# Kernel tuning notes

Hardware: AMD Instinct MI355X
Metric: run time of the kernel (lower is better)

Reference implementation:

```python
import jax, jax.numpy as jnp
import numpy as np

DIM = 1024
HIDDEN = 4096
N_EXPERTS = 8
K = 2
TEMP = 1.0


def setup_inputs() -> dict:
    key = jax.random.key(0)
    ks = jax.random.split(key, 7)
    s = 0.02
    x = jax.random.normal(ks[0], (4, 2048, DIM), dtype=jnp.float32)
    router_w = jax.random.normal(ks[1], (N_EXPERTS, DIM), dtype=jnp.float32) * s
    router_b = jnp.zeros((N_EXPERTS,), dtype=jnp.float32)
    # Expert(dim, hidden, 'swiglu'): fc1: dim -> 2*hidden, fc2: hidden -> dim
    w1 = jax.random.normal(ks[2], (N_EXPERTS, 2 * HIDDEN, DIM), dtype=jnp.float32) * s
    b1 = jnp.zeros((N_EXPERTS, 2 * HIDDEN), dtype=jnp.float32)
    w2 = jax.random.normal(ks[3], (N_EXPERTS, DIM, HIDDEN), dtype=jnp.float32) * s
    b2 = jnp.zeros((N_EXPERTS, DIM), dtype=jnp.float32)
    return {"x": x, "router_w": router_w, "router_b": router_b,
            "w1": w1, "b1": b1, "w2": w2, "b2": b2}


def _expert_ffn(xf, wa, ba, wb, bb):
    # xf: [T, dim]; swiglu FFN
    h = xf @ wa.T + ba                       # [T, 2*hidden]
    h1, h2 = jnp.split(h, 2, axis=-1)
    h = jax.nn.silu(h1) * h2                 # [T, hidden]
    return h @ wb.T + bb                     # [T, dim]


def reference(x, router_w, router_b, w1, b1, w2, b2):
    b, t, d = x.shape
    logits = (x @ router_w.T + router_b) / TEMP          # [b, t, E]
    topk_val, topk_idx = jax.lax.top_k(logits, K)        # [b, t, K]
    weights = jax.nn.softmax(topk_val, axis=-1)          # [b, t, K]

    xf = x.reshape(-1, d)                                # [T, dim]
    # Compute every expert on all tokens (dense reference for irregular dispatch)
    outs = jax.vmap(_expert_ffn, in_axes=(None, 0, 0, 0, 0))(xf, w1, b1, w2, b2)  # [E, T, dim]
    outs = jnp.transpose(outs, (1, 0, 2))                # [T, E, dim]

    idx = topk_idx.reshape(-1, K)                        # [T, K]
    gathered = jnp.take_along_axis(outs, idx[:, :, None], axis=1)  # [T, K, dim]
    combined = (gathered * weights.reshape(-1, K, 1)).sum(axis=1)  # [T, dim]
    return combined.reshape(b, t, d)
```

## Files before the change

kernel.cpp:

```cpp
#include <hip/hip_runtime.h>

#define T_TOK 8192
#define DIMX 1024
#define HID 4096
#define NE 8
#define TP (T_TOK * 2)
#define PADR 128
#define BK 64

typedef unsigned short ushort_t;
typedef __attribute__((ext_vector_type(4))) float f32x4;
typedef __attribute__((ext_vector_type(8))) short bf16x8;

__device__ __forceinline__ ushort_t f2bf(float f) {
    unsigned u = __float_as_uint(f);
    u += 0x7FFFu + ((u >> 16) & 1u);
    return (ushort_t)(u >> 16);
}
__device__ __forceinline__ float b2f(ushort_t h) {
    return __uint_as_float(((unsigned)h) << 16);
}

__device__ __forceinline__ void gload_lds16(const void* g, void* l) {
    __builtin_amdgcn_global_load_lds((const __attribute__((address_space(1))) void*)g,
                                     (__attribute__((address_space(3))) void*)l, 16, 0, 0);
}

__device__ __forceinline__ f32x4 mfma16(bf16x8 a, bf16x8 b, f32x4 c) {
    return __builtin_amdgcn_mfma_f32_16x16x32_bf16(a, b, c, 0, 0, 0);
}


__global__ void zero_kernel(int* p) {
    if (threadIdx.x < 16) p[threadIdx.x] = 0;
}

__global__ __launch_bounds__(256) void router_kernel(
    const float* __restrict__ x, const float* __restrict__ rw, const float* __restrict__ rb,
    int* __restrict__ counts, int* __restrict__ topk_idx, float* __restrict__ topk_w)
{
    __shared__ float s_rw[NE * DIMX];
    int tid = threadIdx.x;
    for (int i = tid * 4; i < NE * DIMX; i += 1024) {
        float4 v = *(const float4*)(rw + i);
        *(float4*)(s_rw + i) = v;
    }
    __syncthreads();
    int lane = tid & 63, wid = tid >> 6;
    int t = blockIdx.x * 4 + wid;
    const float* xr = x + (size_t)t * DIMX;
    float acc[NE];
#pragma unroll
    for (int e = 0; e < NE; e++) acc[e] = 0.f;
    for (int j = 0; j < DIMX; j += 64) {
        float xv = xr[j + lane];
#pragma unroll
        for (int e = 0; e < NE; e++) acc[e] += xv * s_rw[e * DIMX + j + lane];
    }
#pragma unroll
    for (int e = 0; e < NE; e++) {
#pragma unroll
        for (int off = 32; off > 0; off >>= 1) acc[e] += __shfl_xor(acc[e], off, 64);
    }
    if (lane == 0) {
        float v[NE];
#pragma unroll
        for (int e = 0; e < NE; e++) v[e] = acc[e] + rb[e];
        int i0 = 0; float b0 = v[0];
#pragma unroll
        for (int e = 1; e < NE; e++) if (v[e] > b0) { b0 = v[e]; i0 = e; }
        int i1 = -1; float b1v = -1e30f;
#pragma unroll
        for (int e = 0; e < NE; e++) if (e != i0 && v[e] > b1v) { b1v = v[e]; i1 = e; }
        float ex = __expf(b1v - b0);
        float inv = 1.f / (1.f + ex);
        topk_idx[t * 2]     = i0;  topk_idx[t * 2 + 1] = i1;
        topk_w[t * 2]       = inv; topk_w[t * 2 + 1]   = ex * inv;
        atomicAdd(&counts[i0], 1); atomicAdd(&counts[i1], 1);
    }
}

__global__ void prefix_kernel(const int* __restrict__ counts, int* __restrict__ offsets) {
    if (threadIdx.x == 0 && blockIdx.x == 0) {
        int s = 0;
        for (int e = 0; e < NE; e++) { offsets[e] = s; s += counts[e]; }
    }
}

__global__ __launch_bounds__(256) void scatter_kernel(
    const int* __restrict__ topk_idx, const float* __restrict__ topk_w,
    const int* __restrict__ offsets, int* __restrict__ cursor,
    int* __restrict__ tok_of, float* __restrict__ w_of, int* __restrict__ slot_of)
{
    int i = blockIdx.x * 256 + threadIdx.x;
    int e = topk_idx[i];
    int pos = offsets[e] + atomicAdd(&cursor[e], 1);
    tok_of[pos] = i >> 1;
    w_of[pos] = topk_w[i];
    slot_of[i] = pos;
}


__global__ __launch_bounds__(256) void cvt_kernel(
    const float* __restrict__ src, ushort_t* __restrict__ dst, int n8)
{
    int i = blockIdx.x * 256 + threadIdx.x;
    if (i >= n8) return;
    float4 a = ((const float4*)src)[i * 2];
    float4 b = ((const float4*)src)[i * 2 + 1];
    ushort4 lo = make_ushort4(f2bf(a.x), f2bf(a.y), f2bf(a.z), f2bf(a.w));
    ushort4 hi = make_ushort4(f2bf(b.x), f2bf(b.y), f2bf(b.z), f2bf(b.w));
    ((ushort4*)dst)[i * 2] = lo;
    ((ushort4*)dst)[i * 2 + 1] = hi;
}

__global__ __launch_bounds__(256) void gather_kernel(
    const float* __restrict__ x, const int* __restrict__ tok_of, ushort_t* __restrict__ Xp)
{
    int pos = blockIdx.x;
    int t = tok_of[pos];
    int i = threadIdx.x;
    float4 v = ((const float4*)(x + (size_t)t * DIMX))[i];
    ushort4 o = make_ushort4(f2bf(v.x), f2bf(v.y), f2bf(v.z), f2bf(v.w));
    ((ushort4*)(Xp + (size_t)pos * DIMX))[i] = o;
}

__global__ __launch_bounds__(256, 2) void fc1_kernel(
    const ushort_t* __restrict__ Xp, const ushort_t* __restrict__ w1b,
    const float* __restrict__ b1,
    const int* __restrict__ counts, const int* __restrict__ offsets,
    ushort_t* __restrict__ H)
{
    const int e = blockIdx.z, mt = blockIdx.y, nt = blockIdx.x;
    const int cnt = counts[e];
    if (mt * 128 >= cnt) return;
    const int base = offsets[e] + mt * 128;
    int rows_valid = cnt - mt * 128; if (rows_valid > 128) rows_valid = 128;

    __shared__ ushort_t As[128 * BK];
    __shared__ ushort_t Bs1[64 * BK];
    __shared__ ushort_t Bs2[64 * BK];

    const int tid = threadIdx.x, lane = tid & 63, wid = tid >> 6;
    const int wave_m = wid >> 1, wave_n = wid & 1;

    const ushort_t* Ag  = Xp + (size_t)base * DIMX;
    const ushort_t* B1g = w1b + ((size_t)e * 2 * HID + (size_t)nt * 64) * DIMX;
    const ushort_t* B2g = B1g + (size_t)HID * DIMX;

    const ushort_t* agp[4]; ushort_t* alp[4];
#pragma unroll
    for (int i = 0; i < 4; i++) {
        int s = wid * 4 + i;
        int r = s * 8 + (lane >> 3);
        int c = (lane & 7) ^ (r & 7);
        agp[i] = Ag + (size_t)r * DIMX + c * 8;
        alp[i] = As + s * 512 + lane * 8;
    }
    const ushort_t* bgp[4]; ushort_t* blp[4];
#pragma unroll
    for (int i = 0; i < 2; i++) {
        int s = wid * 2 + i;
        int r = s * 8 + (lane >> 3);
        int c = (lane & 7) ^ (r & 7);
        bgp[i]     = B1g + (size_t)r * DIMX + c * 8;
        blp[i]     = Bs1 + s * 512 + lane * 8;
        bgp[2 + i] = B2g + (size_t)r * DIMX + c * 8;
        blp[2 + i] = Bs2 + s * 512 + lane * 8;
    }

    f32x4 acc1[4][2], acc2[4][2];
#pragma unroll
    for (int mf = 0; mf < 4; mf++)
#pragma unroll
        for (int nf = 0; nf < 2; nf++) {
            acc1[mf][nf] = (f32x4){0.f, 0.f, 0.f, 0.f};
            acc2[mf][nf] = (f32x4){0.f, 0.f, 0.f, 0.f};
        }

    const int q = lane >> 4, rA = lane & 15;
    for (int ko = 0; ko < DIMX / BK; ko++) {
#pragma unroll
        for (int i = 0; i < 4; i++) gload_lds16(agp[i], alp[i]);
#pragma unroll
        for (int i = 0; i < 4; i++) gload_lds16(bgp[i], blp[i]);
#pragma unroll
        for (int i = 0; i < 4; i++) { agp[i] += BK; bgp[i] += BK; }
        __syncthreads();

        bf16x8 af[4][2], bf1[2][2], bf2[2][2];
#pragma unroll
        for (int mf = 0; mf < 4; mf++) {
            int r = wave_m * 64 + mf * 16 + rA;
            const ushort_t* rp = As + r * BK;
            af[mf][0] = *(const bf16x8*)(rp + ((q    ) ^ (r & 7)) * 8);
            af[mf][1] = *(const bf16x8*)(rp + ((q + 4) ^ (r & 7)) * 8);
        }
#pragma unroll
        for (int nf = 0; nf < 2; nf++) {
            int r = wave_n * 32 + nf * 16 + rA;
            const ushort_t* rp1 = Bs1 + r * BK;
            const ushort_t* rp2 = Bs2 + r * BK;
            bf1[nf][0] = *(const bf16x8*)(rp1 + ((q    ) ^ (r & 7)) * 8);
            bf1[nf][1] = *(const bf16x8*)(rp1 + ((q + 4) ^ (r & 7)) * 8);
            bf2[nf][0] = *(const bf16x8*)(rp2 + ((q    ) ^ (r & 7)) * 8);
            bf2[nf][1] = *(const bf16x8*)(rp2 + ((q + 4) ^ (r & 7)) * 8);
        }
#pragma unroll
        for (int mf = 0; mf < 4; mf++)
#pragma unroll
            for (int nf = 0; nf < 2; nf++) {
                acc1[mf][nf] = mfma16(af[mf][0], bf1[nf][0], acc1[mf][nf]);
                acc1[mf][nf] = mfma16(af[mf][1], bf1[nf][1], acc1[mf][nf]);
                acc2[mf][nf] = mfma16(af[mf][0], bf2[nf][0], acc2[mf][nf]);
                acc2[mf][nf] = mfma16(af[mf][1], bf2[nf][1], acc2[mf][nf]);
            }
        __syncthreads();
    }

    const float* b1p = b1 + (size_t)e * 2 * HID + (size_t)nt * 64;
#pragma unroll
    for (int mf = 0; mf < 4; mf++) {
#pragma unroll
        for (int nf = 0; nf < 2; nf++) {
            int col = wave_n * 32 + nf * 16 + rA;
            float bb1 = b1p[col];
            float bb2 = b1p[HID + col];
#pragma unroll
            for (int rr = 0; rr < 4; rr++) {
                int row = wave_m * 64 + mf * 16 + q * 4 + rr;
                if (row < rows_valid) {
                    float v1 = acc1[mf][nf][rr] + bb1;
                    float v2 = acc2[mf][nf][rr] + bb2;
                    float hv = v1 * v2 / (1.f + __expf(-v1));
                    H[(size_t)(base + row) * HID + (size_t)nt * 64 + col] = f2bf(hv);
                }
            }
        }
    }
}

__global__ __launch_bounds__(256, 2) void fc2_kernel(
    const ushort_t* __restrict__ H, const ushort_t* __restrict__ w2b,
    const float* __restrict__ b2,
    const int* __restrict__ counts, const int* __restrict__ offsets,
    const float* __restrict__ w_of, ushort_t* __restrict__ Os)
{
    const int e = blockIdx.z, mt = blockIdx.x, nt = blockIdx.y;
    const int cnt = counts[e];
    if (mt * 128 >= cnt) return;
    const int base = offsets[e] + mt * 128;
    int rows_valid = cnt - mt * 128; if (rows_valid > 128) rows_valid = 128;

    __shared__ ushort_t As[128 * BK];
    __shared__ ushort_t Bs[128 * BK];

    const int tid = threadIdx.x, lane = tid & 63, wid = tid >> 6;
    const int wave_m = wid >> 1, wave_n = wid & 1;

    const ushort_t* Ag = H + (size_t)base * HID;
    const ushort_t* Bg = w2b + ((size_t)e * DIMX + (size_t)nt * 128) * HID;

    const ushort_t* agp[4]; ushort_t* alp[4];
    const ushort_t* bgp[4]; ushort_t* blp[4];
#pragma unroll
    for (int i = 0; i < 4; i++) {
        int s = wid * 4 + i;
        int r = s * 8 + (lane >> 3);
        int c = (lane & 7) ^ (r & 7);
        agp[i] = Ag + (size_t)r * HID + c * 8;
        alp[i] = As + s * 512 + lane * 8;
        bgp[i] = Bg + (size_t)r * HID + c * 8;
        blp[i] = Bs + s * 512 + lane * 8;
    }

    f32x4 acc[4][4];
#pragma unroll
    for (int mf = 0; mf < 4; mf++)
#pragma unroll
        for (int nf = 0; nf < 4; nf++) acc[mf][nf] = (f32x4){0.f, 0.f, 0.f, 0.f};

    const int q = lane >> 4, rA = lane & 15;
    for (int ko = 0; ko < HID / BK; ko++) {
#pragma unroll
        for (int i = 0; i < 4; i++) gload_lds16(agp[i], alp[i]);
#pragma unroll
        for (int i = 0; i < 4; i++) gload_lds16(bgp[i], blp[i]);
#pragma unroll
        for (int i = 0; i < 4; i++) { agp[i] += BK; bgp[i] += BK; }
        __syncthreads();

        bf16x8 af[4][2], bfr[4][2];
#pragma unroll
        for (int mf = 0; mf < 4; mf++) {
            int r = wave_m * 64 + mf * 16 + rA;
            const ushort_t* rp = As + r * BK;
            af[mf][0] = *(const bf16x8*)(rp + ((q    ) ^ (r & 7)) * 8);
            af[mf][1] = *(const bf16x8*)(rp + ((q + 4) ^ (r & 7)) * 8);
        }
#pragma unroll
        for (int nf = 0; nf < 4; nf++) {
            int r = wave_n * 64 + nf * 16 + rA;
            const ushort_t* rp = Bs + r * BK;
            bfr[nf][0] = *(const bf16x8*)(rp + ((q    ) ^ (r & 7)) * 8);
            bfr[nf][1] = *(const bf16x8*)(rp + ((q + 4) ^ (r & 7)) * 8);
        }
#pragma unroll
        for (int mf = 0; mf < 4; mf++)
#pragma unroll
            for (int nf = 0; nf < 4; nf++) {
                acc[mf][nf] = mfma16(af[mf][0], bfr[nf][0], acc[mf][nf]);
                acc[mf][nf] = mfma16(af[mf][1], bfr[nf][1], acc[mf][nf]);
            }
        __syncthreads();
    }

    const float* b2p = b2 + (size_t)e * DIMX + (size_t)nt * 128;
#pragma unroll
    for (int mf = 0; mf < 4; mf++) {
#pragma unroll
        for (int rr = 0; rr < 4; rr++) {
            int row = wave_m * 64 + mf * 16 + q * 4 + rr;
            if (row < rows_valid) {
                float wv = w_of[base + row];
#pragma unroll
                for (int nf = 0; nf < 4; nf++) {
                    int col = wave_n * 64 + nf * 16 + rA;
                    float val = (acc[mf][nf][rr] + b2p[col]) * wv;
                    Os[(size_t)(base + row) * DIMX + (size_t)nt * 128 + col] = f2bf(val);
                }
            }
        }
    }
}

__global__ __launch_bounds__(256) void combine_kernel(
    const ushort_t* __restrict__ Os, const int* __restrict__ slot_of, float* __restrict__ out)
{
    int t = blockIdx.x;
    int p0 = slot_of[t * 2], p1 = slot_of[t * 2 + 1];
    int i = threadIdx.x;
    ushort4 a = ((const ushort4*)(Os + (size_t)p0 * DIMX))[i];
    ushort4 b = ((const ushort4*)(Os + (size_t)p1 * DIMX))[i];
    float4 o;
    o.x = b2f(a.x) + b2f(b.x);
    o.y = b2f(a.y) + b2f(b.y);
    o.z = b2f(a.z) + b2f(b.z);
    o.w = b2f(a.w) + b2f(b.w);
    ((float4*)(out + (size_t)t * DIMX))[i] = o;
}


extern "C" void kernel_launch(void* const* d_in, const int* in_sizes, int n_in,
                              void* d_out, int out_size, void* d_ws, size_t ws_size,
                              hipStream_t stream) {
    (void)in_sizes; (void)n_in; (void)out_size; (void)ws_size;
    const float* x  = (const float*)d_in[0];
    const float* rw = (const float*)d_in[1];
    const float* rb = (const float*)d_in[2];
    const float* w1 = (const float*)d_in[3];
    const float* b1 = (const float*)d_in[4];
    const float* w2 = (const float*)d_in[5];
    const float* b2 = (const float*)d_in[6];
    float* out = (float*)d_out;

    char* p = (char*)d_ws;
    ushort_t* w1b = (ushort_t*)p; p += (size_t)NE * 2 * HID * DIMX * 2;
    ushort_t* w2b = (ushort_t*)p; p += (size_t)NE * DIMX * HID * 2;
    ushort_t* Xp  = (ushort_t*)p; p += (size_t)(TP + PADR) * DIMX * 2;
    ushort_t* Hb  = (ushort_t*)p; p += (size_t)(TP + PADR) * HID * 2;
    ushort_t* Os  = (ushort_t*)p; p += (size_t)TP * DIMX * 2;
    int* ints     = (int*)p;      p += 24 * sizeof(int);
    int*   counts  = ints;
    int*   cursor  = ints + 8;
    int*   offsets = ints + 16;
    int*   topk_idx = (int*)p;   p += (size_t)TP * 4;
    float* topk_w   = (float*)p; p += (size_t)TP * 4;
    int*   tok_of   = (int*)p;   p += (size_t)TP * 4;
    float* w_of     = (float*)p; p += (size_t)TP * 4;
    int*   slot_of  = (int*)p;   p += (size_t)TP * 4;

    zero_kernel<<<1, 64, 0, stream>>>(counts);
    router_kernel<<<T_TOK / 4, 256, 0, stream>>>(x, rw, rb, counts, topk_idx, topk_w);
    prefix_kernel<<<1, 64, 0, stream>>>(counts, offsets);
    scatter_kernel<<<TP / 256, 256, 0, stream>>>(topk_idx, topk_w, offsets, cursor,
                                                 tok_of, w_of, slot_of);
    cvt_kernel<<<(NE * 2 * HID * DIMX / 8 + 255) / 256, 256, 0, stream>>>(w1, w1b, NE * 2 * HID * DIMX / 8);
    cvt_kernel<<<(NE * DIMX * HID / 8 + 255) / 256, 256, 0, stream>>>(w2, w2b, NE * DIMX * HID / 8);
    gather_kernel<<<TP, 256, 0, stream>>>(x, tok_of, Xp);

    fc1_kernel<<<dim3(HID / 64, 32, NE), 256, 0, stream>>>(Xp, w1b, b1, counts, offsets, Hb);
    fc2_kernel<<<dim3(32, DIMX / 128, NE), 256, 0, stream>>>(Hb, w2b, b2, counts, offsets, w_of, Os);
    combine_kernel<<<T_TOK, 256, 0, stream>>>(Os, slot_of, out);
}
```

Before: 1.356 ms.

## Consolidate MoE dispatch kernels, merge weight conversion, split fc1 launch, alias output buffer

Removes the zero and scatter/gather kernels. Routing counts now come from a single-block histogram over topk_idx, and a fused per-token scatter+gather kernel converts each x row once and writes it to both expert slots. The two weight-conversion launches become one grid-stride kernel with 16-byte stores. fc1 is split into two half-width launches, the epilogue bounds check is skipped for full tiles, and Os reuses the Xp buffer to save workspace. The single-block histogram serializes the counting work, and the fc1 split adds a launch without reducing work.

```diff
diff --git a/kernel.cpp b/kernel.cpp
--- a/kernel.cpp
+++ b/kernel.cpp
@@ -11,6 +11,7 @@
 typedef unsigned short ushort_t;
 typedef __attribute__((ext_vector_type(4))) float f32x4;
 typedef __attribute__((ext_vector_type(8))) short bf16x8;
+typedef __attribute__((ext_vector_type(8))) unsigned short u16x8;
 
 __device__ __forceinline__ ushort_t f2bf(float f) {
     unsigned u = __float_as_uint(f);
@@ -31,13 +32,9 @@
 }
 
 
-__global__ void zero_kernel(int* p) {
-    if (threadIdx.x < 16) p[threadIdx.x] = 0;
-}
-
 __global__ __launch_bounds__(256) void router_kernel(
     const float* __restrict__ x, const float* __restrict__ rw, const float* __restrict__ rb,
-    int* __restrict__ counts, int* __restrict__ topk_idx, float* __restrict__ topk_w)
+    int* __restrict__ topk_idx, float* __restrict__ topk_w)
 {
     __shared__ float s_rw[NE * DIMX];
     int tid = threadIdx.x;
@@ -76,62 +73,87 @@
         float inv = 1.f / (1.f + ex);
         topk_idx[t * 2]     = i0;  topk_idx[t * 2 + 1] = i1;
         topk_w[t * 2]       = inv; topk_w[t * 2 + 1]   = ex * inv;
-        atomicAdd(&counts[i0], 1); atomicAdd(&counts[i1], 1);
-    }
-}
-
-__global__ void prefix_kernel(const int* __restrict__ counts, int* __restrict__ offsets) {
-    if (threadIdx.x == 0 && blockIdx.x == 0) {
+    }
+}
+
+__global__ __launch_bounds__(256) void prefix_kernel(
+    const int* __restrict__ topk_idx, int* __restrict__ counts,
+    int* __restrict__ offsets, int* __restrict__ cursor)
+{
+    __shared__ int hist[NE * 256];
+    int tid = threadIdx.x;
+    int loc[NE];
+#pragma unroll
+    for (int e = 0; e < NE; e++) loc[e] = 0;
+    for (int i = tid; i < TP; i += 256) loc[topk_idx[i]]++;
+#pragma unroll
+    for (int e = 0; e < NE; e++) hist[e * 256 + tid] = loc[e];
+    __syncthreads();
+    if (tid < NE) {
+        int s = 0;
+        for (int j = 0; j < 256; j++) s += hist[tid * 256 + j];
+        counts[tid] = s;
+        cursor[tid] = 0;
+    }
+    __syncthreads();
+    if (tid == 0) {
         int s = 0;
         for (int e = 0; e < NE; e++) { offsets[e] = s; s += counts[e]; }
     }
 }
 
-__global__ __launch_bounds__(256) void scatter_kernel(
-    const int* __restrict__ topk_idx, const float* __restrict__ topk_w,
-    const int* __restrict__ offsets, int* __restrict__ cursor,
-    int* __restrict__ tok_of, float* __restrict__ w_of, int* __restrict__ slot_of)
-{
-    int i = blockIdx.x * 256 + threadIdx.x;
-    int e = topk_idx[i];
-    int pos = offsets[e] + atomicAdd(&cursor[e], 1);
-    tok_of[pos] = i >> 1;
-    w_of[pos] = topk_w[i];
-    slot_of[i] = pos;
-}
-
-
-__global__ __launch_bounds__(256) void cvt_kernel(
-    const float* __restrict__ src, ushort_t* __restrict__ dst, int n8)
-{
-    int i = blockIdx.x * 256 + threadIdx.x;
-    if (i >= n8) return;
-    float4 a = ((const float4*)src)[i * 2];
-    float4 b = ((const float4*)src)[i * 2 + 1];
-    ushort4 lo = make_ushort4(f2bf(a.x), f2bf(a.y), f2bf(a.z), f2bf(a.w));
-    ushort4 hi = make_ushort4(f2bf(b.x), f2bf(b.y), f2bf(b.z), f2bf(b.w));
-    ((ushort4*)dst)[i * 2] = lo;
-    ((ushort4*)dst)[i * 2 + 1] = hi;
-}
-
-__global__ __launch_bounds__(256) void gather_kernel(
-    const float* __restrict__ x, const int* __restrict__ tok_of, ushort_t* __restrict__ Xp)
-{
-    int pos = blockIdx.x;
-    int t = tok_of[pos];
+__global__ __launch_bounds__(256) void sg_kernel(
+    const float* __restrict__ x, const int* __restrict__ topk_idx,
+    const float* __restrict__ topk_w, const int* __restrict__ offsets,
+    int* __restrict__ cursor, ushort_t* __restrict__ Xp,
+    float* __restrict__ w_of, int* __restrict__ slot_of)
+{
+    __shared__ int s_pos[2];
+    int t = blockIdx.x;
+    if (threadIdx.x == 0) {
+        int e0 = topk_idx[2 * t], e1 = topk_idx[2 * t + 1];
+        int p0 = offsets[e0] + atomicAdd(&cursor[e0], 1);
+        int p1 = offsets[e1] + atomicAdd(&cursor[e1], 1);
+        s_pos[0] = p0; s_pos[1] = p1;
+        w_of[p0] = topk_w[2 * t]; w_of[p1] = topk_w[2 * t + 1];
+        slot_of[2 * t] = p0; slot_of[2 * t + 1] = p1;
+    }
+    __syncthreads();
+    int p0 = s_pos[0], p1 = s_pos[1];
     int i = threadIdx.x;
     float4 v = ((const float4*)(x + (size_t)t * DIMX))[i];
     ushort4 o = make_ushort4(f2bf(v.x), f2bf(v.y), f2bf(v.z), f2bf(v.w));
-    ((ushort4*)(Xp + (size_t)pos * DIMX))[i] = o;
+    ((ushort4*)(Xp + (size_t)p0 * DIMX))[i] = o;
+    ((ushort4*)(Xp + (size_t)p1 * DIMX))[i] = o;
+}
+
+
+__global__ __launch_bounds__(256) void cvt_kernel(
+    const float* __restrict__ w1, ushort_t* __restrict__ w1d,
+    const float* __restrict__ w2, ushort_t* __restrict__ w2d)
+{
+    const int n8_w1 = NE * 2 * HID * DIMX / 8;
+    const int n8_tot = n8_w1 + NE * DIMX * HID / 8;
+    int stride = gridDim.x * 256;
+    for (int i = blockIdx.x * 256 + threadIdx.x; i < n8_tot; i += stride) {
+        const float* src; ushort_t* dst; int j;
+        if (i < n8_w1) { src = w1; dst = w1d; j = i; }
+        else           { src = w2; dst = w2d; j = i - n8_w1; }
+        float4 a = ((const float4*)src)[j * 2];
+        float4 b = ((const float4*)src)[j * 2 + 1];
+        u16x8 o = { f2bf(a.x), f2bf(a.y), f2bf(a.z), f2bf(a.w),
+                    f2bf(b.x), f2bf(b.y), f2bf(b.z), f2bf(b.w) };
+        ((u16x8*)dst)[j] = o;
+    }
 }
 
 __global__ __launch_bounds__(256, 2) void fc1_kernel(
     const ushort_t* __restrict__ Xp, const ushort_t* __restrict__ w1b,
     const float* __restrict__ b1,
     const int* __restrict__ counts, const int* __restrict__ offsets,
-    ushort_t* __restrict__ H)
-{
-    const int e = blockIdx.z, mt = blockIdx.y, nt = blockIdx.x;
+    ushort_t* __restrict__ H, const int nt0)
+{
+    const int e = blockIdx.z, mt = blockIdx.y, nt = blockIdx.x + nt0;
     const int cnt = counts[e];
     if (mt * 128 >= cnt) return;
     const int base = offsets[e] + mt * 128;
@@ -219,6 +241,7 @@
     }
 
     const float* b1p = b1 + (size_t)e * 2 * HID + (size_t)nt * 64;
+    const bool full = (rows_valid == 128);
 #pragma unroll
     for (int mf = 0; mf < 4; mf++) {
 #pragma unroll
@@ -229,7 +252,7 @@
 #pragma unroll
             for (int rr = 0; rr < 4; rr++) {
                 int row = wave_m * 64 + mf * 16 + q * 4 + rr;
-                if (row < rows_valid) {
+                if (full || row < rows_valid) {
                     float v1 = acc1[mf][nf][rr] + bb1;
                     float v2 = acc2[mf][nf][rr] + bb2;
                     float hv = v1 * v2 / (1.f + __expf(-v1));
@@ -316,12 +339,13 @@
     }
 
     const float* b2p = b2 + (size_t)e * DIMX + (size_t)nt * 128;
+    const bool full = (rows_valid == 128);
 #pragma unroll
     for (int mf = 0; mf < 4; mf++) {
 #pragma unroll
         for (int rr = 0; rr < 4; rr++) {
             int row = wave_m * 64 + mf * 16 + q * 4 + rr;
-            if (row < rows_valid) {
+            if (full || row < rows_valid) {
                 float wv = w_of[base + row];
 #pragma unroll
                 for (int nf = 0; nf < 4; nf++) {
@@ -369,27 +393,24 @@
     ushort_t* w2b = (ushort_t*)p; p += (size_t)NE * DIMX * HID * 2;
     ushort_t* Xp  = (ushort_t*)p; p += (size_t)(TP + PADR) * DIMX * 2;
     ushort_t* Hb  = (ushort_t*)p; p += (size_t)(TP + PADR) * HID * 2;
-    ushort_t* Os  = (ushort_t*)p; p += (size_t)TP * DIMX * 2;
     int* ints     = (int*)p;      p += 24 * sizeof(int);
     int*   counts  = ints;
     int*   cursor  = ints + 8;
     int*   offsets = ints + 16;
     int*   topk_idx = (int*)p;   p += (size_t)TP * 4;
     float* topk_w   = (float*)p; p += (size_t)TP * 4;
-    int*   tok_of   = (int*)p;   p += (size_t)TP * 4;
     float* w_of     = (float*)p; p += (size_t)TP * 4;
     int*   slot_of  = (int*)p;   p += (size_t)TP * 4;
-
-    zero_kernel<<<1, 64, 0, stream>>>(counts);
-    router_kernel<<<T_TOK / 4, 256, 0, stream>>>(x, rw, rb, counts, topk_idx, topk_w);
-    prefix_kernel<<<1, 64, 0, stream>>>(counts, offsets);
-    scatter_kernel<<<TP / 256, 256, 0, stream>>>(topk_idx, topk_w, offsets, cursor,
-                                                 tok_of, w_of, slot_of);
-    cvt_kernel<<<(NE * 2 * HID * DIMX / 8 + 255) / 256, 256, 0, stream>>>(w1, w1b, NE * 2 * HID * DIMX / 8);
-    cvt_kernel<<<(NE * DIMX * HID / 8 + 255) / 256, 256, 0, stream>>>(w2, w2b, NE * DIMX * HID / 8);
-    gather_kernel<<<TP, 256, 0, stream>>>(x, tok_of, Xp);
-
-    fc1_kernel<<<dim3(HID / 64, 32, NE), 256, 0, stream>>>(Xp, w1b, b1, counts, offsets, Hb);
+    ushort_t* Os = Xp;
+
+    router_kernel<<<T_TOK / 4, 256, 0, stream>>>(x, rw, rb, topk_idx, topk_w);
+    prefix_kernel<<<1, 256, 0, stream>>>(topk_idx, counts, offsets, cursor);
+    sg_kernel<<<T_TOK, 256, 0, stream>>>(x, topk_idx, topk_w, offsets, cursor,
+                                         Xp, w_of, slot_of);
+    cvt_kernel<<<2048, 256, 0, stream>>>(w1, w1b, w2, w2b);
+
+    fc1_kernel<<<dim3(32, 32, NE), 256, 0, stream>>>(Xp, w1b, b1, counts, offsets, Hb, 0);
+    fc1_kernel<<<dim3(32, 32, NE), 256, 0, stream>>>(Xp, w1b, b1, counts, offsets, Hb, 32);
     fc2_kernel<<<dim3(32, DIMX / 128, NE), 256, 0, stream>>>(Hb, w2b, b2, counts, offsets, w_of, Os);
     combine_kernel<<<T_TOK, 256, 0, stream>>>(Os, slot_of, out);
 }
```

Result: faster. 1.319 ms (-2.8%).
